# Kernel optimization log

Measured on AMD Instinct MI355X. Metric: run time of the kernel, lower is better.

## Reference

```python
import jax, jax.numpy as jnp
from jax import lax
import numpy as np

FEAT_W = 52      # feature map width/height
IMG_W = 210      # input image width/height
SUB = IMG_W // FEAT_W  # = 4, sub_sample stride
N_ANCHOR = 9
NMS_THRESH = 0.7
PRE_NMS = 12000
POST_NMS = 2000
MIN_SIZE = 16.0


def make_anchors():
    # Faithful vectorization of generateAnchors: outer loop over ctr_x, inner over ctr_y,
    # then c unpacked as (ctr_y, ctr_x) = (x_val, y_val); ratios outer, scales inner.
    vals = (np.arange(SUB, (FEAT_W + 1) * SUB, SUB) - SUB // 2).astype(np.float64)  # 2,6,...,210
    cy = np.repeat(vals, FEAT_W)   # outer loop value -> anchor ctr_y
    cx = np.tile(vals, FEAT_W)     # inner loop value -> anchor ctr_x
    ratios = np.array([0.5, 1.0, 2.0])
    scales = np.array([4.0, 8.0, 16.0])
    h = (SUB * scales[None, :] * np.sqrt(ratios[:, None])).reshape(-1)      # (9,)
    w = (SUB * scales[None, :] * np.sqrt(1.0 / ratios[:, None])).reshape(-1)
    a = np.stack([cy[:, None] - h / 2.0, cx[:, None] - w / 2.0,
                  cy[:, None] + h / 2.0, cx[:, None] + w / 2.0], axis=-1)   # (2704, 9, 4)
    return a.reshape(-1, 4).astype(np.float32)  # (24336, 4) as [y1,x1,y2,x2]

_ANCHORS = jnp.asarray(make_anchors())


def _conv(x, w, b):
    y = lax.conv_general_dilated(x, w, (1, 1), 'SAME',
                                 dimension_numbers=('NCHW', 'OIHW', 'NCHW'))
    return y + b[None, :, None, None]


def propose_regions(locs, obj):
    # locs: (1, 24336, 4); obj: (1, 24336)
    anc = _ANCHORS
    ah = anc[:, 2] - anc[:, 0]
    aw = anc[:, 3] - anc[:, 1]
    acy = anc[:, 0] + 0.5 * ah
    acx = anc[:, 1] + 0.5 * aw
    l = locs[0]
    s = obj[0]
    cy = l[:, 0] * ah + acy
    cx = l[:, 1] * aw + acx
    hh = jnp.exp(l[:, 2]) * ah
    ww = jnp.exp(l[:, 3]) * aw
    roi = jnp.stack([cy - 0.5 * hh, cx - 0.5 * ww,
                     cy + 0.5 * hh, cx + 0.5 * ww], axis=1)
    roi = jnp.clip(roi, 0.0, float(IMG_W))
    hs = roi[:, 2] - roi[:, 0]
    ws = roi[:, 3] - roi[:, 1]
    valid = (hs >= MIN_SIZE) & (ws >= MIN_SIZE)
    # min_size filter folded into score masking; invalid boxes start suppressed
    masked = jnp.where(valid, s, -jnp.inf)
    order = jnp.argsort(-masked)[:PRE_NMS]
    boxes = roi[order]          # (PRE_NMS, 4) sorted by descending score
    v = valid[order]
    sgb = lax.stop_gradient(boxes)
    areas = (sgb[:, 3] - sgb[:, 1] + 1.0) * (sgb[:, 2] - sgb[:, 0] + 1.0)
    idxs = jnp.arange(PRE_NMS)

    def body(supp, i):
        b = sgb[i]
        yy1 = jnp.maximum(b[0], sgb[:, 0])
        xx1 = jnp.maximum(b[1], sgb[:, 1])
        yy2 = jnp.minimum(b[2], sgb[:, 2])
        xx2 = jnp.minimum(b[3], sgb[:, 3])
        inter = jnp.maximum(0.0, xx2 - xx1 + 1.0) * jnp.maximum(0.0, yy2 - yy1 + 1.0)
        iou = inter / (areas[i] + areas - inter)
        new = supp | ((iou > NMS_THRESH) & (idxs > i))
        return jnp.where(supp[i], supp, new), None

    supp, _ = lax.scan(body, ~v, idxs)  # greedy sequential NMS, fixed length
    keep = ~supp
    rank = jnp.cumsum(keep.astype(jnp.int32)) - 1
    write = keep & (rank < POST_NMS)
    tgt = jnp.where(write, rank, POST_NMS)  # overflow/dropped rows go to scrap slot
    out = jnp.zeros((POST_NMS + 1, 4), boxes.dtype).at[tgt].set(
        jnp.where(write[:, None], boxes, 0.0))
    return out[:POST_NMS]  # (2000, 4), zero-padded


def _forward(x, conv1_w, conv1_b, reg_w, reg_b, cls_w, cls_b):
    h = _conv(x, conv1_w, conv1_b)        # (1,256,52,52), no activation (as in source)
    reg = _conv(h, reg_w, reg_b)          # (1,36,52,52)
    cls = _conv(h, cls_w, cls_b)          # (1,18,52,52)
    locs = jnp.transpose(reg, (0, 2, 3, 1)).reshape(1, -1, 4)          # (1,24336,4)
    cls_t = jnp.transpose(cls, (0, 2, 3, 1))                            # (1,52,52,18)
    obj = cls_t.reshape(1, FEAT_W, FEAT_W, N_ANCHOR, 2)[..., 1].reshape(1, -1)
    cls_scores = cls_t.reshape(1, -1, 2)                                # (1,24336,2)
    rois = propose_regions(locs, obj)
    return rois, locs, cls_scores, obj


def setup_inputs() -> dict:
    key = jax.random.key(0)
    ks = jax.random.split(key, 4)
    x = jax.random.normal(ks[0], (1, 256, FEAT_W, FEAT_W), jnp.float32)
    conv1_w = 0.01 * jax.random.normal(ks[1], (256, 256, 3, 3), jnp.float32)
    conv1_b = jnp.zeros((256,), jnp.float32)
    reg_w = 0.01 * jax.random.normal(ks[2], (N_ANCHOR * 4, 256, 1, 1), jnp.float32)
    reg_b = jnp.zeros((N_ANCHOR * 4,), jnp.float32)
    cls_w = 0.01 * jax.random.normal(ks[3], (N_ANCHOR * 2, 256, 1, 1), jnp.float32)
    cls_b = jnp.zeros((N_ANCHOR * 2,), jnp.float32)
    return {"x": x, "conv1_w": conv1_w, "conv1_b": conv1_b,
            "reg_w": reg_w, "reg_b": reg_b, "cls_w": cls_w, "cls_b": cls_b}


def reference(x, conv1_w, conv1_b, reg_w, reg_b, cls_w, cls_b):
    rois, locs, cls_scores, obj = _forward(x, conv1_w, conv1_b, reg_w, reg_b, cls_w, cls_b)
    return (rois, locs, cls_scores, obj, cls_scores)
```

## Files before the change

### kernel.cpp

```cpp
#include <hip/hip_runtime.h>

typedef unsigned long long u64;
typedef unsigned int u32;

#define FEAT 52
#define NPIX 2704
#define NANC 24336
#define PRE  12000
#define POST 2000
#define ROWW 192
#define PADW 54
#define PADS 2916

#define ROIS_OFF 0
#define LOCS_OFF 8000
#define CLS_OFF  105344
#define OBJ_OFF  154016
#define CLS2_OFF 178352

#define OFF_W64   0ull
#define OFF_H64   4718592ull
#define OFF_REG64 10256384ull
#define OFF_SC64  11035136ull
#define OFF_ROI64 11229824ull
#define OFF_KEYS  12008576ull
#define OFF_SBOX  12270720ull
#define OFF_SAREA 12663936ull
#define OFF_SUPP  12762240ull
#define OFF_MASK  12763776ull
#define OFF_XPAD  OFF_MASK
#define OFF_H64B  (OFF_MASK + 2985984ull)

__global__ __launch_bounds__(256) void k_prepx(const float* __restrict__ x,
                                               float* __restrict__ xpad) {
    int t = blockIdx.x * 256 + threadIdx.x;
    int ci = t / PADS, pos = t % PADS;
    int iy = pos / PADW, ix = pos % PADW;
    float v = 0.f;
    if (iy >= 1 && iy <= 52 && ix >= 1 && ix <= 52)
        v = x[ci * NPIX + (iy - 1) * FEAT + (ix - 1)];
    xpad[t] = v;
}

__global__ __launch_bounds__(256) void k_prepw(const float* __restrict__ w,
                                               double* __restrict__ w64) {
    int t = blockIdx.x * 256 + threadIdx.x;
    int j = t & 3;
    int r = t >> 2;
    int k = r % 9;
    int r2 = r / 9;
    int ci = r2 & 255;
    int g = r2 >> 8;
    w64[t] = (double)w[(((g * 4 + j) * 256) + ci) * 9 + k];
}

__global__ __launch_bounds__(256) void k_conv3(const float* __restrict__ xpad,
                                               const double* __restrict__ w64,
                                               const float* __restrict__ b,
                                               double* __restrict__ h64,
                                               double* __restrict__ h64b) {
    const int p = blockIdx.x * 256 + threadIdx.x;
    const int o0 = blockIdx.y * 4;
    const int half = blockIdx.z;
    if (p >= NPIX) return;
    const int y = p / FEAT, xq = p % FEAT;
    double a0, a1, a2, a3;
    if (half == 0) {
        a0 = (double)b[o0+0]; a1 = (double)b[o0+1];
        a2 = (double)b[o0+2]; a3 = (double)b[o0+3];
    } else {
        a0 = a1 = a2 = a3 = 0.0;
    }
    const int c0 = half << 7;
    const float* xb = xpad + (size_t)c0 * PADS + y * PADW + xq;
    const double* wb = w64 + (size_t)blockIdx.y * 9216 + c0 * 36;
    #pragma unroll 2
    for (int ci = 0; ci < 128; ++ci) {
        float f0 = xb[0],   f1 = xb[1],   f2 = xb[2];
        float f3 = xb[54],  f4 = xb[55],  f5 = xb[56];
        float f6 = xb[108], f7 = xb[109], f8 = xb[110];
        double xv[9];
        xv[0]=(double)f0; xv[1]=(double)f1; xv[2]=(double)f2;
        xv[3]=(double)f3; xv[4]=(double)f4; xv[5]=(double)f5;
        xv[6]=(double)f6; xv[7]=(double)f7; xv[8]=(double)f8;
        const double* wr = wb + ci * 36;
        #pragma unroll
        for (int k = 0; k < 9; ++k) {
            a0 += xv[k] * wr[4*k+0];
            a1 += xv[k] * wr[4*k+1];
            a2 += xv[k] * wr[4*k+2];
            a3 += xv[k] * wr[4*k+3];
        }
        xb += PADS;
    }
    double* ho = (half == 0) ? h64 : h64b;
    ho[(o0+0)*NPIX + p] = a0;
    ho[(o0+1)*NPIX + p] = a1;
    ho[(o0+2)*NPIX + p] = a2;
    ho[(o0+3)*NPIX + p] = a3;
}

__global__ __launch_bounds__(64) void k_conv1(const double* __restrict__ h64,
                                              const double* __restrict__ h64b,
                                              const float* __restrict__ regw,
                                              const float* __restrict__ regb,
                                              const float* __restrict__ clsw,
                                              const float* __restrict__ clsb,
                                              float* __restrict__ out,
                                              double* __restrict__ reg64,
                                              double* __restrict__ score64) {
    const int g = blockIdx.y;
    const int p = blockIdx.x * 64 + threadIdx.x;
    if (p >= NPIX) return;
    const bool isreg = (g < 4);
    const float* wbase = isreg ? (regw + g * 9 * 256) : (clsw + (g - 4) * 9 * 256);
    const float* bbase = isreg ? (regb + g * 9)       : (clsb + (g - 4) * 9);
    double acc[9];
    #pragma unroll
    for (int j = 0; j < 9; ++j) acc[j] = (double)bbase[j];
    #pragma unroll 4
    for (int ci = 0; ci < 256; ++ci) {
        double h = h64[ci * NPIX + p] + h64b[ci * NPIX + p];
        #pragma unroll
        for (int j = 0; j < 9; ++j)
            acc[j] += h * (double)wbase[j * 256 + ci];
    }
    #pragma unroll
    for (int j = 0; j < 9; ++j) {
        int oc = g * 9 + j;
        float v = (float)acc[j];
        if (isreg) {
            out[LOCS_OFF + p*36 + oc] = v;
            reg64[p*36 + oc] = acc[j];
        } else {
            int c = oc - 36;
            out[CLS_OFF  + p*18 + c] = v;
            out[CLS2_OFF + p*18 + c] = v;
            if (c & 1) {
                out[OBJ_OFF + p*9 + (c >> 1)] = v;
                score64[p*9 + (c >> 1)] = acc[j];
            }
        }
    }
}

__global__ __launch_bounds__(256) void k_decode(const double* __restrict__ reg64,
                                                const double* __restrict__ score64,
                                                double* __restrict__ roi64,
                                                u64* __restrict__ keys) {
    int t = blockIdx.x * 256 + threadIdx.x;
    if (t >= NANC) { keys[t] = ~0ull; return; }
    int pos = t / 9, a = t % 9;
    int py = pos / FEAT, px = pos % FEAT;
    int ri = a / 3, si = a % 3;
    double rat = (ri == 0) ? 0.5 : (ri == 1 ? 1.0 : 2.0);
    double scl = (si == 0) ? 4.0 : (si == 1 ? 8.0 : 16.0);
    double hA = 4.0 * scl * sqrt(rat);
    double wA = 4.0 * scl * sqrt(1.0 / rat);
    double cy0 = 4.0 * py + 2.0, cx0 = 4.0 * px + 2.0;
    float y1f = (float)(cy0 - hA / 2.0), x1f = (float)(cx0 - wA / 2.0);
    float y2f = (float)(cy0 + hA / 2.0), x2f = (float)(cx0 + wA / 2.0);
    double ah = (double)y2f - (double)y1f, aw = (double)x2f - (double)x1f;
    double acy = (double)y1f + 0.5 * ah, acx = (double)x1f + 0.5 * aw;
    double l0 = reg64[4*t+0], l1 = reg64[4*t+1], l2 = reg64[4*t+2], l3 = reg64[4*t+3];
    double cy = l0 * ah + acy, cx = l1 * aw + acx;
    double hh = exp(l2) * ah,  ww = exp(l3) * aw;
    double r0 = fmin(fmax(cy - 0.5*hh, 0.0), 210.0);
    double r1 = fmin(fmax(cx - 0.5*ww, 0.0), 210.0);
    double r2 = fmin(fmax(cy + 0.5*hh, 0.0), 210.0);
    double r3 = fmin(fmax(cx + 0.5*ww, 0.0), 210.0);
    roi64[4*t+0] = r0; roi64[4*t+1] = r1; roi64[4*t+2] = r2; roi64[4*t+3] = r3;
    bool valid = (r2 - r0 >= 16.0) && (r3 - r1 >= 16.0);
    double m = valid ? score64[t] : -__builtin_huge_val();
    long long ll = __double_as_longlong(m);
    u64 u = (u64)ll;
    u64 mono = (ll < 0) ? ~u : (u ^ 0x8000000000000000ull);
    keys[t] = ((~mono) & 0xFFFFFFFFFFFF0000ull) | (u64)t;
}

__global__ __launch_bounds__(1024) void k_sortA(u64* __restrict__ keys) {
    __shared__ u64 s[8192];
    const int base = blockIdx.x * 8192;
    for (int t = threadIdx.x; t < 8192; t += 1024) s[t] = keys[base + t];
    __syncthreads();
    for (int k = 2; k <= 8192; k <<= 1) {
        for (int j = k >> 1; j > 0; j >>= 1) {
            for (int q = threadIdx.x; q < 4096; q += 1024) {
                int i = ((q & ~(j-1)) << 1) | (q & (j-1));
                int l = i | j;
                bool asc = (((base + i) & k) == 0);
                u64 A = s[i], B = s[l];
                bool sw = asc ? (A > B) : (A < B);
                if (sw) { s[i] = B; s[l] = A; }
            }
            __syncthreads();
        }
    }
    for (int t = threadIdx.x; t < 8192; t += 1024) keys[base + t] = s[t];
}

__global__ __launch_bounds__(1024) void k_sortB(u64* __restrict__ keys, int k) {
    __shared__ u64 s[8192];
    const int base = blockIdx.x * 8192;
    for (int t = threadIdx.x; t < 8192; t += 1024) s[t] = keys[base + t];
    __syncthreads();
    for (int j = 4096; j > 0; j >>= 1) {
        for (int q = threadIdx.x; q < 4096; q += 1024) {
            int i = ((q & ~(j-1)) << 1) | (q & (j-1));
            int l = i | j;
            bool asc = (((base + i) & k) == 0);
            u64 A = s[i], B = s[l];
            bool sw = asc ? (A > B) : (A < B);
            if (sw) { s[i] = B; s[l] = A; }
        }
        __syncthreads();
    }
    for (int t = threadIdx.x; t < 8192; t += 1024) keys[base + t] = s[t];
}

__global__ __launch_bounds__(256) void k_sortG(u64* __restrict__ keys, int k, int j) {
    int t = blockIdx.x * 256 + threadIdx.x;
    int i = ((t & ~(j-1)) << 1) | (t & (j-1));
    int l = i | j;
    bool asc = ((i & k) == 0);
    u64 A = keys[i], B = keys[l];
    bool sw = asc ? (A > B) : (A < B);
    if (sw) { keys[i] = B; keys[l] = A; }
}

__global__ __launch_bounds__(256) void k_gather(const u64* __restrict__ keys,
                                                const double* __restrict__ roi64,
                                                double* __restrict__ sbox,
                                                double* __restrict__ sarea,
                                                u64* __restrict__ suppinit) {
    int p = blockIdx.x * 256 + threadIdx.x;
    bool sup = true;
    if (p < PRE) {
        int idx = (int)(keys[p] & 0xFFFFull);
        double b0 = roi64[4*idx+0], b1 = roi64[4*idx+1];
        double b2 = roi64[4*idx+2], b3 = roi64[4*idx+3];
        sbox[4*p+0] = b0; sbox[4*p+1] = b1; sbox[4*p+2] = b2; sbox[4*p+3] = b3;
        sarea[p] = (b3 - b1 + 1.0) * (b2 - b0 + 1.0);
        sup = !((b2 - b0 >= 16.0) && (b3 - b1 >= 16.0));
    } else {
        sbox[4*p+0] = 0.0; sbox[4*p+1] = 0.0; sbox[4*p+2] = 0.0; sbox[4*p+3] = 0.0;
        sarea[p] = 1.0;
    }
    u64 ball = __ballot(sup);
    if ((threadIdx.x & 63) == 0) suppinit[p >> 6] = ball;
}

__global__ __launch_bounds__(256) void k_mask(const double* __restrict__ sbox,
                                              const double* __restrict__ sarea,
                                              u64* __restrict__ mask) {
    const int jt = blockIdx.x, it = blockIdx.y;
    const int ib = it * 64, jb0 = jt * 1024;
    if (jb0 + 1023 <= ib) {
        for (int t = threadIdx.x; t < 1024; t += 256) {
            int ti = t >> 4, w = t & 15;
            int i = ib + ti;
            if (i < PRE) mask[(size_t)i * ROWW + jt*16 + w] = 0ull;
        }
        return;
    }
    __shared__ double jbx[4096];
    __shared__ double jar[1024];
    for (int t = threadIdx.x; t < 4096; t += 256) jbx[t] = sbox[(size_t)jb0*4 + t];
    for (int t = threadIdx.x; t < 1024; t += 256) jar[t] = sarea[jb0 + t];
    __syncthreads();
    int ti = threadIdx.x >> 2;
    int i = ib + ti;
    if (i >= PRE) return;
    double iy1 = sbox[4*i+0], ix1 = sbox[4*i+1], iy2 = sbox[4*i+2], ix2 = sbox[4*i+3];
    double iar = sarea[i];
    for (int w = (threadIdx.x & 3); w < 16; w += 4) {
        u64 bits = 0ull;
        int q0 = w * 64;
        for (int l = 0; l < 64; ++l) {
            int q = q0 + l;
            double jy1 = jbx[4*q+0], jx1 = jbx[4*q+1], jy2 = jbx[4*q+2], jx2 = jbx[4*q+3];
            double yy1 = fmax(iy1, jy1), xx1 = fmax(ix1, jx1);
            double yy2 = fmin(iy2, jy2), xx2 = fmin(ix2, jx2);
            double iw = fmax(xx2 - xx1 + 1.0, 0.0);
            double ih = fmax(yy2 - yy1 + 1.0, 0.0);
            double inter = iw * ih;
            bool s = ((jb0 + q) > i) && (inter > 0.7 * (iar + jar[q] - inter));
            bits |= ((u64)s) << l;
        }
        mask[(size_t)i * ROWW + jt*16 + w] = bits;
    }
}

__device__ inline u64 rdl64(u64 v, int l) {
    u32 lo = (u32)__builtin_amdgcn_readlane((int)(u32)v, l);
    u32 hi = (u32)__builtin_amdgcn_readlane((int)(u32)(v >> 32), l);
    return ((u64)hi << 32) | (u64)lo;
}
#define RFL64(lo, hi) ( ((u64)(u32)__builtin_amdgcn_readfirstlane((int)(hi)) << 32) \
                      | (u64)(u32)__builtin_amdgcn_readfirstlane((int)(lo)) )

__global__ __launch_bounds__(512) void k_scan(const u64* __restrict__ mask,
                                              const u64* __restrict__ suppinit,
                                              const double* __restrict__ sbox,
                                              float* __restrict__ rois) {
    __shared__ u64 dbuf[2][4608];
    __shared__ u32 keptLDS[POST];
    __shared__ u32 supp8[2][16];
    __shared__ int rankS, doneS;
    const int tid = threadIdx.x;
    const u32* suppinit32 = (const u32*)suppinit;

    if (tid < 16)                 supp8[0][tid]      = suppinit32[tid];
    else if (tid < 32)            supp8[1][tid - 16] = suppinit32[tid];
    if (tid == 0) { rankS = 0; doneS = 0; }
    for (int q = tid; q < 4096; q += 512) {
        int r = q >> 3, w = q & 7;
        dbuf[0][r*9 + w] = (r < PRE) ? mask[(size_t)r * ROWW + w] : 0ull;
    }
    __syncthreads();

    int rank0 = 0;
    for (int c = 0; c < 24; ++c) {
        const int nc = c + 1;
        const int cb = c & 1, nb = nc & 1;
        if (tid < 64) {
            const int lane = tid;
            u64 i0 = RFL64(supp8[cb][0],  supp8[cb][1]);
            u64 i1 = RFL64(supp8[cb][2],  supp8[cb][3]);
            u64 i2 = RFL64(supp8[cb][4],  supp8[cb][5]);
            u64 i3 = RFL64(supp8[cb][6],  supp8[cb][7]);
            u64 i4 = RFL64(supp8[cb][8],  supp8[cb][9]);
            u64 i5 = RFL64(supp8[cb][10], supp8[cb][11]);
            u64 i6 = RFL64(supp8[cb][12], supp8[cb][13]);
            u64 i7 = RFL64(supp8[cb][14], supp8[cb][15]);
            u64 a0=0,a1=0,a2=0,a3=0,a4=0,a5=0,a6=0,a7=0;
            int rk = __builtin_amdgcn_readfirstlane(rankS);
            bool dn = false;
#define GROUP(G)                                                                \
            if (!dn) {                                                          \
                u64 z = ~(i##G | a##G);                                         \
                if (z) {                                                        \
                    u64 r0=0,r1=0,r2=0,r3=0,r4=0,r5=0,r6=0,r7=0;                \
                    if ((z >> lane) & 1ull) {                                   \
                        const u64* rowp = &dbuf[cb][(G*64 + lane)*9];           \
                        r0=rowp[0]; r1=rowp[1]; r2=rowp[2]; r3=rowp[3];         \
                        r4=rowp[4]; r5=rowp[5]; r6=rowp[6]; r7=rowp[7];         \
                    }                                                           \
                    u64 keptm = 0;                                              \
                    while (z) {                                                 \
                        int bpos = (int)__builtin_ctzll(z);                     \
                        u64 q0=rdl64(r0,bpos), q1=rdl64(r1,bpos);               \
                        u64 q2=rdl64(r2,bpos), q3=rdl64(r3,bpos);               \
                        u64 q4=rdl64(r4,bpos), q5=rdl64(r5,bpos);               \
                        u64 q6=rdl64(r6,bpos), q7=rdl64(r7,bpos);               \
                        keptm |= (1ull << bpos);                                \
                        z &= ~(1ull << bpos) & ~q##G;                           \
                        a0|=q0; a1|=q1; a2|=q2; a3|=q3;                         \
                        a4|=q4; a5|=q5; a6|=q6; a7|=q7;                         \
                    }                                                           \
                    int pc = __builtin_popcountll(keptm);                       \
                    int navail = POST - rk;                                     \
                    int mylot = __builtin_amdgcn_mbcnt_hi((u32)(keptm >> 32),   \
                                 __builtin_amdgcn_mbcnt_lo((u32)keptm, 0));     \
                    if (((keptm >> lane) & 1) && mylot < navail)                \
                        keptLDS[rk + mylot] = (u32)(c*512 + G*64 + lane);       \
                    if (pc >= navail) { rk = POST; dn = true; }                 \
                    else rk += pc;                                              \
                }                                                               \
            }
            GROUP(0) GROUP(1) GROUP(2) GROUP(3)
            GROUP(4) GROUP(5) GROUP(6) GROUP(7)
#undef GROUP
            if (lane == 0) { rankS = rk; if (dn) doneS = 1; }
        } else if (tid < 256) {
            if (nc < 24) {
                for (int q = tid - 64; q < 4096; q += 192) {
                    int r = q >> 3, w = q & 7;
                    int i = nc*512 + r;
                    dbuf[nb][r*9 + w] = (i < PRE) ? mask[(size_t)i * ROWW + nc*8 + w] : 0ull;
                }
            }
        } else {
            if (nc < 24 && rank0 > 0) {
                u64 acc[8] = {0,0,0,0,0,0,0,0};
                for (int k = tid - 256; k < rank0; k += 256) {
                    const u64* rp = mask + (size_t)keptLDS[k] * ROWW + nc*8;
                    #pragma unroll
                    for (int w = 0; w < 8; ++w) acc[w] |= rp[w];
                }
                #pragma unroll
                for (int w = 0; w < 8; ++w) {
                    u64 v = acc[w];
                    #pragma unroll
                    for (int s = 1; s < 64; s <<= 1)
                        v |= (u64)__shfl_xor((unsigned long long)v, s, 64);
                    if ((tid & 63) == 0) {
                        if ((u32)v)         atomicOr(&supp8[nb][2*w],   (u32)v);
                        if ((u32)(v >> 32)) atomicOr(&supp8[nb][2*w+1], (u32)(v >> 32));
                    }
                }
            }
        }
        __syncthreads();
        if (doneS) break;
        if (nc >= 24) break;
        const int rk1 = rankS;
        {
            int w = tid & 7;
            u64 acc = 0;
            for (int k = rank0 + (tid >> 3); k < rk1; k += 64)
                acc |= mask[(size_t)keptLDS[k] * ROWW + nc*8 + w];
            if ((u32)acc)         atomicOr(&supp8[nb][2*w],   (u32)acc);
            if ((u32)(acc >> 32)) atomicOr(&supp8[nb][2*w+1], (u32)(acc >> 32));
            if (tid < 16) supp8[cb][tid] = (c + 2 < 24) ? suppinit32[(c+2)*16 + tid] : 0u;
        }
        rank0 = rk1;
        __syncthreads();
    }
    __syncthreads();
    const int R = rankS;
    for (int r = tid; r < POST; r += 512) {
        if (r < R) {
            int p = (int)keptLDS[r];
            rois[4*r+0] = (float)sbox[4*p+0];
            rois[4*r+1] = (float)sbox[4*p+1];
            rois[4*r+2] = (float)sbox[4*p+2];
            rois[4*r+3] = (float)sbox[4*p+3];
        }
    }
}

extern "C" void kernel_launch(void* const* d_in, const int* in_sizes, int n_in,
                              void* d_out, int out_size, void* d_ws, size_t ws_size,
                              hipStream_t stream) {
    const float* x    = (const float*)d_in[0];
    const float* w1   = (const float*)d_in[1];
    const float* b1   = (const float*)d_in[2];
    const float* regw = (const float*)d_in[3];
    const float* regb = (const float*)d_in[4];
    const float* clsw = (const float*)d_in[5];
    const float* clsb = (const float*)d_in[6];
    float* out = (float*)d_out;

    char* ws = (char*)d_ws;
    double* w64    = (double*)(ws + OFF_W64);
    double* h64    = (double*)(ws + OFF_H64);
    double* reg64  = (double*)(ws + OFF_REG64);
    double* sc64   = (double*)(ws + OFF_SC64);
    double* roi64  = (double*)(ws + OFF_ROI64);
    u64*    keys   = (u64*)   (ws + OFF_KEYS);
    double* sbox   = (double*)(ws + OFF_SBOX);
    double* sarea  = (double*)(ws + OFF_SAREA);
    u64*    supp0  = (u64*)   (ws + OFF_SUPP);
    u64*    maskp  = (u64*)   (ws + OFF_MASK);
    float*  xpad   = (float*) (ws + OFF_XPAD);
    double* h64b   = (double*)(ws + OFF_H64B);

    hipMemsetAsync(d_out, 0, 8000 * sizeof(float), stream);

    k_prepx<<<2916, 256, 0, stream>>>(x, xpad);
    k_prepw<<<2304, 256, 0, stream>>>(w1, w64);
    k_conv3<<<dim3(11, 64, 2), 256, 0, stream>>>(xpad, w64, b1, h64, h64b);
    k_conv1<<<dim3(43, 6), 64, 0, stream>>>(h64, h64b, regw, regb, clsw, clsb, out, reg64, sc64);
    k_decode<<<128, 256, 0, stream>>>(reg64, sc64, roi64, keys);

    k_sortA<<<4, 1024, 0, stream>>>(keys);
    k_sortG<<<64, 256, 0, stream>>>(keys, 16384, 8192);
    k_sortB<<<4, 1024, 0, stream>>>(keys, 16384);
    k_sortG<<<64, 256, 0, stream>>>(keys, 32768, 16384);
    k_sortG<<<64, 256, 0, stream>>>(keys, 32768, 8192);
    k_sortB<<<4, 1024, 0, stream>>>(keys, 32768);

    k_gather<<<48, 256, 0, stream>>>(keys, roi64, sbox, sarea, supp0);
    k_mask<<<dim3(12, 188), 256, 0, stream>>>(sbox, sarea, maskp);
    k_scan<<<1, 512, 0, stream>>>(maskp, supp0, sbox, out + ROIS_OFF);
}
```

Before: 635.1 us.

## Rewrite NMS scan inner loop in scalar asm and merge prep kernels

The serial greedy NMS scan now walks each 64-bit candidate group as two 32-bit halves using an inline-assembly scalar loop (s_ff1, v_readlane, s_andn2). Only the group's own mask word is read per kept box, and the later groups' accumulators are updated afterwards from the kept set rather than all eight words on every iteration. This is meant to shorten the single-wave critical path. The padding and weight-conversion prep kernels are also merged into one launch to save a kernel launch. The inline asm adds fragility and depends on correct register-class constraints.

```diff
diff --git a/kernel.cpp b/kernel.cpp
--- a/kernel.cpp
+++ b/kernel.cpp
@@ -31,27 +31,29 @@
 #define OFF_XPAD  OFF_MASK
 #define OFF_H64B  (OFF_MASK + 2985984ull)
 
-__global__ __launch_bounds__(256) void k_prepx(const float* __restrict__ x,
-                                               float* __restrict__ xpad) {
-    int t = blockIdx.x * 256 + threadIdx.x;
-    int ci = t / PADS, pos = t % PADS;
-    int iy = pos / PADW, ix = pos % PADW;
-    float v = 0.f;
-    if (iy >= 1 && iy <= 52 && ix >= 1 && ix <= 52)
-        v = x[ci * NPIX + (iy - 1) * FEAT + (ix - 1)];
-    xpad[t] = v;
-}
-
-__global__ __launch_bounds__(256) void k_prepw(const float* __restrict__ w,
-                                               double* __restrict__ w64) {
-    int t = blockIdx.x * 256 + threadIdx.x;
-    int j = t & 3;
-    int r = t >> 2;
-    int k = r % 9;
-    int r2 = r / 9;
-    int ci = r2 & 255;
-    int g = r2 >> 8;
-    w64[t] = (double)w[(((g * 4 + j) * 256) + ci) * 9 + k];
+__global__ __launch_bounds__(256) void k_prep(const float* __restrict__ x,
+                                              float* __restrict__ xpad,
+                                              const float* __restrict__ w,
+                                              double* __restrict__ w64) {
+    int b = blockIdx.x;
+    if (b < 2916) {
+        int t = b * 256 + threadIdx.x;
+        int ci = t / PADS, pos = t % PADS;
+        int iy = pos / PADW, ix = pos % PADW;
+        float v = 0.f;
+        if (iy >= 1 && iy <= 52 && ix >= 1 && ix <= 52)
+            v = x[ci * NPIX + (iy - 1) * FEAT + (ix - 1)];
+        xpad[t] = v;
+    } else {
+        int t = (b - 2916) * 256 + threadIdx.x;
+        int j = t & 3;
+        int r = t >> 2;
+        int k = r % 9;
+        int r2 = r / 9;
+        int ci = r2 & 255;
+        int g = r2 >> 8;
+        w64[t] = (double)w[(((g * 4 + j) * 256) + ci) * 9 + k];
+    }
 }
 
 __global__ __launch_bounds__(256) void k_conv3(const float* __restrict__ xpad,
@@ -296,8 +298,65 @@
     u32 hi = (u32)__builtin_amdgcn_readlane((int)(u32)(v >> 32), l);
     return ((u64)hi << 32) | (u64)lo;
 }
-#define RFL64(lo, hi) ( ((u64)(u32)__builtin_amdgcn_readfirstlane((int)(hi)) << 32) \
-                      | (u64)(u32)__builtin_amdgcn_readfirstlane((int)(lo)) )
+
+#define SCAN_HALF(ZVAR, KMVAR, RSRC, OFF)                                       \
+    { u32 bp_, ln_, q_;                                                         \
+      asm volatile(                                                             \
+        "s_cmp_lg_u32 %[z], 0\n\t"                                              \
+        "s_cbranch_scc0 Lend%=\n\t"                                             \
+        "Lloop%=:\n\t"                                                          \
+        "s_ff1_i32_b32 %[bp], %[z]\n\t"                                         \
+        "s_add_i32 %[ln], %[bp], %[off]\n\t"                                    \
+        "v_readlane_b32 %[q], %[r], %[ln]\n\t"                                  \
+        "s_bitset1_b32 %[km], %[bp]\n\t"                                        \
+        "s_bitset0_b32 %[z], %[bp]\n\t"                                         \
+        "s_andn2_b32 %[z], %[z], %[q]\n\t"                                      \
+        "s_cbranch_scc1 Lloop%=\n\t"                                            \
+        "Lend%=:"                                                               \
+        : [z]"+s"(ZVAR), [km]"+s"(KMVAR), [bp]"=&s"(bp_), [ln]"=&s"(ln_),       \
+          [q]"=&s"(q_)                                                          \
+        : [r]"v"(RSRC), [off]"i"(OFF)                                           \
+        : "scc"); }
+
+#define UPD(W) a##W |= rdl64(r##W, ln_);
+
+#define RFL(expr) ((u32)__builtin_amdgcn_readfirstlane((int)(expr)))
+
+#define GROUPX(G, UPDS)                                                         \
+    if (!dn) {                                                                  \
+        u32 zlo = RFL(~(s8[2*(G)]   | (u32)(a##G)));                            \
+        u32 zhi = RFL(~(s8[2*(G)+1] | (u32)(a##G >> 32)));                      \
+        u64 zl64 = ((u64)zhi << 32) | (u64)zlo;                                 \
+        u64 r0=0,r1=0,r2=0,r3=0,r4=0,r5=0,r6=0,r7=0;                            \
+        if ((zl64 >> lane) & 1ull) {                                            \
+            const u64* rowp = &dbuf[cb][((G)*64 + lane)*9];                     \
+            r0=rowp[0]; r1=rowp[1]; r2=rowp[2]; r3=rowp[3];                     \
+            r4=rowp[4]; r5=rowp[5]; r6=rowp[6]; r7=rowp[7];                     \
+        }                                                                       \
+        u32 kmlo = 0, kmhi = 0;                                                 \
+        if (zlo) SCAN_HALF(zlo, kmlo, (u32)(r##G), 0)                           \
+        { u32 t0 = kmlo, sup_ = 0;                                              \
+          while (t0) { int l2 = __builtin_ctz(t0); t0 &= t0 - 1;                \
+              sup_ |= (u32)__builtin_amdgcn_readlane((int)(u32)(r##G >> 32), l2); } \
+          zhi &= ~sup_; }                                                       \
+        if (zhi) SCAN_HALF(zhi, kmhi, (u32)(r##G >> 32), 32)                    \
+        u64 km64 = ((u64)kmhi << 32) | (u64)kmlo;                               \
+        if (km64) {                                                             \
+            int pc = __builtin_popcountll(km64);                                \
+            int navail = POST - rk;                                             \
+            int mylot = __builtin_amdgcn_mbcnt_hi((u32)(km64 >> 32),            \
+                         __builtin_amdgcn_mbcnt_lo((u32)km64, 0));              \
+            if (((km64 >> lane) & 1) && mylot < navail)                         \
+                keptLDS[rk + mylot] = (u32)(c*512 + (G)*64 + lane);             \
+            if (pc >= navail) { rk = POST; dn = true; }                         \
+            else {                                                              \
+                rk += pc;                                                       \
+                u64 t_ = km64;                                                  \
+                while (t_) { int ln_ = __builtin_ctzll(t_); t_ &= t_ - 1;       \
+                             UPDS }                                             \
+            }                                                                   \
+        }                                                                       \
+    }
 
 __global__ __launch_bounds__(512) void k_scan(const u64* __restrict__ mask,
                                               const u64* __restrict__ suppinit,
@@ -325,52 +384,19 @@
         const int cb = c & 1, nb = nc & 1;
         if (tid < 64) {
             const int lane = tid;
-            u64 i0 = RFL64(supp8[cb][0],  supp8[cb][1]);
-            u64 i1 = RFL64(supp8[cb][2],  supp8[cb][3]);
-            u64 i2 = RFL64(supp8[cb][4],  supp8[cb][5]);
-            u64 i3 = RFL64(supp8[cb][6],  supp8[cb][7]);
-            u64 i4 = RFL64(supp8[cb][8],  supp8[cb][9]);
-            u64 i5 = RFL64(supp8[cb][10], supp8[cb][11]);
-            u64 i6 = RFL64(supp8[cb][12], supp8[cb][13]);
-            u64 i7 = RFL64(supp8[cb][14], supp8[cb][15]);
+            const u32* s8 = supp8[cb];
             u64 a0=0,a1=0,a2=0,a3=0,a4=0,a5=0,a6=0,a7=0;
             int rk = __builtin_amdgcn_readfirstlane(rankS);
             bool dn = false;
-#define GROUP(G)                                                                \
-            if (!dn) {                                                          \
-                u64 z = ~(i##G | a##G);                                         \
-                if (z) {                                                        \
-                    u64 r0=0,r1=0,r2=0,r3=0,r4=0,r5=0,r6=0,r7=0;                \
-                    if ((z >> lane) & 1ull) {                                   \
-                        const u64* rowp = &dbuf[cb][(G*64 + lane)*9];           \
-                        r0=rowp[0]; r1=rowp[1]; r2=rowp[2]; r3=rowp[3];         \
-                        r4=rowp[4]; r5=rowp[5]; r6=rowp[6]; r7=rowp[7];         \
-                    }                                                           \
-                    u64 keptm = 0;                                              \
-                    while (z) {                                                 \
-                        int bpos = (int)__builtin_ctzll(z);                     \
-                        u64 q0=rdl64(r0,bpos), q1=rdl64(r1,bpos);               \
-                        u64 q2=rdl64(r2,bpos), q3=rdl64(r3,bpos);               \
-                        u64 q4=rdl64(r4,bpos), q5=rdl64(r5,bpos);               \
-                        u64 q6=rdl64(r6,bpos), q7=rdl64(r7,bpos);               \
-                        keptm |= (1ull << bpos);                                \
-                        z &= ~(1ull << bpos) & ~q##G;                           \
-                        a0|=q0; a1|=q1; a2|=q2; a3|=q3;                         \
-                        a4|=q4; a5|=q5; a6|=q6; a7|=q7;                         \
-                    }                                                           \
-                    int pc = __builtin_popcountll(keptm);                       \
-                    int navail = POST - rk;                                     \
-                    int mylot = __builtin_amdgcn_mbcnt_hi((u32)(keptm >> 32),   \
-                                 __builtin_amdgcn_mbcnt_lo((u32)keptm, 0));     \
-                    if (((keptm >> lane) & 1) && mylot < navail)                \
-                        keptLDS[rk + mylot] = (u32)(c*512 + G*64 + lane);       \
-                    if (pc >= navail) { rk = POST; dn = true; }                 \
-                    else rk += pc;                                              \
-                }                                                               \
-            }
-            GROUP(0) GROUP(1) GROUP(2) GROUP(3)
-            GROUP(4) GROUP(5) GROUP(6) GROUP(7)
-#undef GROUP
+            GROUPX(0, UPD(1)UPD(2)UPD(3)UPD(4)UPD(5)UPD(6)UPD(7))
+            GROUPX(1, UPD(2)UPD(3)UPD(4)UPD(5)UPD(6)UPD(7))
+            GROUPX(2, UPD(3)UPD(4)UPD(5)UPD(6)UPD(7))
+            GROUPX(3, UPD(4)UPD(5)UPD(6)UPD(7))
+            GROUPX(4, UPD(5)UPD(6)UPD(7))
+            GROUPX(5, UPD(6)UPD(7))
+            GROUPX(6, UPD(7))
+            GROUPX(7, (void)ln_;)
+            (void)a7;
             if (lane == 0) { rankS = rk; if (dn) doneS = 1; }
         } else if (tid < 256) {
             if (nc < 24) {
@@ -456,10 +482,9 @@
     float*  xpad   = (float*) (ws + OFF_XPAD);
     double* h64b   = (double*)(ws + OFF_H64B);
 
-    hipMemsetAsync(d_out, 0, 8000 * sizeof(float), stream);
-
-    k_prepx<<<2916, 256, 0, stream>>>(x, xpad);
-    k_prepw<<<2304, 256, 0, stream>>>(w1, w64);
+    (void)hipMemsetAsync(d_out, 0, 8000 * sizeof(float), stream);
+
+    k_prep<<<5220, 256, 0, stream>>>(x, xpad, w1, w64);
     k_conv3<<<dim3(11, 64, 2), 256, 0, stream>>>(xpad, w64, b1, h64, h64b);
     k_conv1<<<dim3(43, 6), 64, 0, stream>>>(h64, h64b, regw, regb, clsw, clsb, out, reg64, sc64);
     k_decode<<<128, 256, 0, stream>>>(reg64, sc64, roi64, keys);
```

New measurement: 690.6 us. +8.7%, slower.
